# Optimization experiments

Measured on AMD Instinct MI355X. Metric: run time of the kernel, lower is better.

## Reference

```python
import jax, jax.numpy as jnp
import numpy as np

NUM_KNOTS = 10
DEGREE = 3
NUM_BASIS = NUM_KNOTS + DEGREE - 1  # 12
IN_FEATURES = 512
OUT_FEATURES = 512


def _interval_bounds():
    # t = linspace(0,1,num_knots); segment i covers [t[max(0,i-deg+1)], t[min(i+1,K-1)])
    t = np.linspace(0.0, 1.0, NUM_KNOTS, dtype=np.float32)
    idx = np.arange(NUM_BASIS)
    lower = t[np.maximum(0, idx - (DEGREE - 1))]
    upper = t[np.minimum(idx + 1, NUM_KNOTS - 1)]
    return jnp.asarray(lower), jnp.asarray(upper)


def setup_inputs() -> dict:
    key = jax.random.key(0)
    kx, kc = jax.random.split(key)
    x = jax.random.uniform(kx, (8, 2048, IN_FEATURES), dtype=jnp.float32)
    # coeffs for spline (i=out, j=in): torch indexes splines[i*in_features+j]
    coeffs = jax.random.normal(kc, (OUT_FEATURES, IN_FEATURES, NUM_BASIS), dtype=jnp.float32)
    return {"x": x, "coeffs": coeffs}


def reference(x, coeffs):
    lower, upper = _interval_bounds()  # [NUM_BASIS] each
    # piecewise-constant basis masks: [b, s, in, NUM_BASIS]
    xe = x[..., None]
    basis = ((xe >= lower) & (xe < upper)).astype(x.dtype)
    # out[b,s,i] = sum_j sum_k basis[b,s,j,k] * coeffs[i,j,k]
    return jnp.einsum("bsjk,ijk->bsi", basis, coeffs)
```

## Files before the change

kernel.cpp:

```cpp
#include <hip/hip_runtime.h>

#define MTOT 16384
#define NFEAT 512
#define KTOT 4608

typedef float f32x4 __attribute__((ext_vector_type(4)));
typedef short s16x8 __attribute__((ext_vector_type(8)));

__device__ __forceinline__ int div9(int c) { return (c * 7282) >> 16; }

#define GLDS(GP, LP) __builtin_amdgcn_global_load_lds( \
    (const __attribute__((address_space(1))) void*)(GP), \
    (__attribute__((address_space(3))) void*)(LP), 16, 0, 0)

__device__ __forceinline__ s16x8 decode_frag(unsigned code) {
  unsigned nb0 = code & 15u, nb1 = code >> 4;
  unsigned p0 = nb0 - 1u, p1 = nb1 - 1u;
  unsigned long long v0 = (nb0 ? 0x3F80ull : 0ull) << ((p0 & 3u) << 4);
  unsigned long long v1 = (nb1 ? 0x3F80ull : 0ull) << ((p1 & 3u) << 4);
  unsigned long long lo = (p0 < 4u ? v0 : 0ull) | (p1 < 4u ? v1 : 0ull);
  unsigned long long hi = (p0 < 4u ? 0ull : v0) | (p1 < 4u ? 0ull : v1);
  union { unsigned long long q[2]; s16x8 v; } u;
  u.q[0] = lo; u.q[1] = hi;
  return u.v;
}

__global__ __launch_bounds__(256) void prep(const float* __restrict__ x,
                                            const float* __restrict__ coeffs,
                                            unsigned char* __restrict__ codeT,
                                            unsigned short* __restrict__ Bmat) {
  __shared__ unsigned char segt[64][68];
  const int bx = blockIdx.x;
  const int tid = threadIdx.x;
  if (bx < 2048) {
    const int i = bx >> 2, q = bx & 3;
    const float* cb = coeffs + (size_t)i * 6144;
#pragma unroll
    for (int p = 0; p < 5; ++p) {
      int kl = p * 256 + tid;
      if (kl < 1152) {
        int k = q * 1152 + kl;
        int j = div9(k), s = k - j * 9;
        float v = cb[j * 12 + s] + cb[j * 12 + s + 1] + cb[j * 12 + s + 2];
        unsigned u = __float_as_uint(v);
        unsigned rn = (u + 0x7FFFu + ((u >> 16) & 1u)) >> 16;
        Bmat[(size_t)i * KTOT + k] = (unsigned short)rn;
      }
    }
  } else {
    const int bb = bx - 2048;
    const int mt = bb >> 3;
    const int jt = bb & 7;
    const int m0 = mt * 64;
    const float4* x4 = (const float4*)x;
    const float T1 = (float)(1.0/9.0), T2 = (float)(2.0/9.0), T3 = (float)(3.0/9.0),
                T4 = (float)(4.0/9.0), T5 = (float)(5.0/9.0), T6 = (float)(6.0/9.0),
                T7 = (float)(7.0/9.0), T8 = (float)(8.0/9.0);
#pragma unroll
    for (int it = 0; it < 4; ++it) {
      int f = it * 256 + tid;
      int m = f >> 4, jq = f & 15;
      float4 v = x4[(size_t)(m0 + m) * 128 + jt * 16 + jq];
      uchar4 sv;
      { float xv = v.x; sv.x = (unsigned char)((xv>=T1)+(xv>=T2)+(xv>=T3)+(xv>=T4)+(xv>=T5)+(xv>=T6)+(xv>=T7)+(xv>=T8)); }
      { float xv = v.y; sv.y = (unsigned char)((xv>=T1)+(xv>=T2)+(xv>=T3)+(xv>=T4)+(xv>=T5)+(xv>=T6)+(xv>=T7)+(xv>=T8)); }
      { float xv = v.z; sv.z = (unsigned char)((xv>=T1)+(xv>=T2)+(xv>=T3)+(xv>=T4)+(xv>=T5)+(xv>=T6)+(xv>=T7)+(xv>=T8)); }
      { float xv = v.w; sv.w = (unsigned char)((xv>=T1)+(xv>=T2)+(xv>=T3)+(xv>=T4)+(xv>=T5)+(xv>=T6)+(xv>=T7)+(xv>=T8)); }
      *(uchar4*)&segt[m][jq * 4] = sv;
    }
    __syncthreads();
#pragma unroll
    for (int p = 0; p < 5; ++p) {
      int u = p * 256 + tid;
      if (u < 1152) {
        int gl = u >> 4, mq = u & 15;
        int c0 = jt * 576 + gl * 8;
        int j0 = div9(c0), j1 = div9(c0 + 7);
        int j0l = j0 - jt * 64, j1l = j1 - jt * 64;
        uchar4 ob;
        unsigned char* pb = (unsigned char*)&ob;
#pragma unroll
        for (int c = 0; c < 4; ++c) {
          int m = mq + c * 16;
          int s0 = segt[m][j0l];
          int pos0 = j0 * 9 + s0 - c0;
          unsigned code = (pos0 >= 0 && pos0 < 8) ? (unsigned)(pos0 + 1) : 0u;
          if (j1 != j0) {
            int s1 = segt[m][j1l];
            int pos1 = j1 * 9 + s1 - c0;
            if (pos1 < 8) code |= (unsigned)(pos1 + 1) << 4;
          }
          pb[c] = (unsigned char)code;
        }
        *(uchar4*)(codeT + (size_t)(jt * 72 + gl) * MTOT + m0 + mq * 4) = ob;
      }
    }
  }
}

__global__ __launch_bounds__(256, 2) void kan_gemm(const unsigned char* __restrict__ codeT,
                                                   const unsigned short* __restrict__ Bmat,
                                                   float* __restrict__ out) {
  __shared__ __align__(16) short Blds[2][2][8192];
  const int tid = threadIdx.x;
  const int lane = tid & 63;
  const int wid = tid >> 6;
  const int mh = wid & 1;
  const int kh = wid >> 1;
  const int lm = lane & 15;
  const int lq = lane >> 4;
  const int bx = blockIdx.x;
  const int mt = bx >> 2;
  const int nt = bx & 3;
  const int m0 = mt * 128, n0 = nt * 128;
  const int mb64 = m0 + mh * 64;

  const unsigned short* gBp = Bmat + (size_t)(n0 + mh * 64 + lm) * KTOT + kh * 2304 + lq * 8;
  const unsigned* gC0 = (const unsigned*)(codeT + (size_t)(kh * 288 + lq) * MTOT + mb64) + lm;
  const unsigned* gC1 = (const unsigned*)(codeT + (size_t)(kh * 288 + 4 + lq) * MTOT + mb64) + lm;

  f32x4 acc[4][8] = {};
  s16x8 bfP[8], bfQ[8];
  unsigned crq[2][2];

#define CRLOAD(SET) do { \
    crq[SET][0] = gC0[0]; crq[SET][1] = gC1[0]; \
    gC0 += 2 * MTOT; gC1 += 2 * MTOT; } while (0)

#define ISSUE_B(SLOT) do { \
    short* dst = &Blds[kh][SLOT][mh * 4096]; \
    GLDS(gBp,                  dst);        \
    GLDS(gBp + 32,             dst + 512);  \
    GLDS(gBp + 16 * KTOT,      dst + 1024); \
    GLDS(gBp + 16 * KTOT + 32, dst + 1536); \
    GLDS(gBp + 32 * KTOT,      dst + 2048); \
    GLDS(gBp + 32 * KTOT + 32, dst + 2560); \
    GLDS(gBp + 48 * KTOT,      dst + 3072); \
    GLDS(gBp + 48 * KTOT + 32, dst + 3584); \
    gBp += 64; } while (0)

#define RD(BF, SLOT, KSD) do { \
    _Pragma("unroll") \
    for (int ns = 0; ns < 8; ++ns) \
      BF[ns] = *(const s16x8*)&Blds[kh][SLOT][(ns * 2 + (KSD)) * 512 + lane * 8]; \
    } while (0)

#define HALF(CRIDX, KSD, BF) do { \
    __builtin_amdgcn_s_setprio(1); \
    unsigned cw_ = crq[CRIDX][KSD]; \
    _Pragma("unroll") \
    for (int ms = 0; ms < 4; ++ms) { \
      s16x8 afv_ = decode_frag((cw_ >> (ms * 8)) & 255u); \
      _Pragma("unroll") \
      for (int ns = 0; ns < 8; ++ns) \
        acc[ms][ns] = __builtin_amdgcn_mfma_f32_16x16x32_bf16(afv_, BF[ns], acc[ms][ns], 0, 0, 0); \
    } \
    __builtin_amdgcn_s_setprio(0); } while (0)

#define VWAIT0() asm volatile("s_waitcnt vmcnt(0)" ::: "memory")
#define BAR()    __builtin_amdgcn_s_barrier()

  CRLOAD(0);
  ISSUE_B(0);
  VWAIT0();
  BAR();
  RD(bfP, 0, 0);

#pragma unroll 1
  for (int tt = 0; tt < 17; ++tt) {
    BAR();
    CRLOAD(1); ISSUE_B(1);
    RD(bfQ, 0, 1);
    HALF(0, 0, bfP);
    VWAIT0();
    BAR();
    RD(bfP, 1, 0);
    HALF(0, 1, bfQ);

    BAR();
    CRLOAD(0); ISSUE_B(0);
    RD(bfQ, 1, 1);
    HALF(1, 0, bfP);
    VWAIT0();
    BAR();
    RD(bfP, 0, 0);
    HALF(1, 1, bfQ);
  }

  BAR();
  CRLOAD(1); ISSUE_B(1);
  RD(bfQ, 0, 1);
  HALF(0, 0, bfP);
  VWAIT0();
  BAR();
  RD(bfP, 1, 0);
  HALF(0, 1, bfQ);

  BAR();
  RD(bfQ, 1, 1);
  HALF(1, 0, bfP);
  HALF(1, 1, bfQ);

  BAR();
  if (kh == 1) {
    float* p = (float*)(&Blds[0][0][0]) + mh * 8192;
#pragma unroll
    for (int ms = 0; ms < 4; ++ms)
#pragma unroll
      for (int ns = 0; ns < 8; ++ns)
#pragma unroll
        for (int rg = 0; rg < 4; ++rg)
          p[((ms * 8 + ns) * 4 + rg) * 64 + lane] = acc[ms][ns][rg];
  }
  __syncthreads();
  if (kh == 0) {
    const float* p = (const float*)(&Blds[0][0][0]) + mh * 8192;
#pragma unroll
    for (int ms = 0; ms < 4; ++ms)
#pragma unroll
      for (int ns = 0; ns < 8; ++ns) {
        int tok = mb64 + ms * 16 + lq * 4;
        int col = n0 + ns * 16 + lm;
        float* op = out + (size_t)tok * NFEAT + col;
#pragma unroll
        for (int rg = 0; rg < 4; ++rg)
          op[(size_t)rg * NFEAT] = acc[ms][ns][rg] + p[((ms * 8 + ns) * 4 + rg) * 64 + lane];
      }
  }
#undef CRLOAD
#undef ISSUE_B
#undef RD
#undef HALF
#undef VWAIT0
#undef BAR
}

extern "C" void kernel_launch(void* const* d_in, const int* in_sizes, int n_in,
                              void* d_out, int out_size, void* d_ws, size_t ws_size,
                              hipStream_t stream) {
  const float* x = (const float*)d_in[0];
  const float* coeffs = (const float*)d_in[1];
  float* out = (float*)d_out;
  unsigned char* codeT = (unsigned char*)d_ws;
  unsigned short* Bmat = (unsigned short*)((char*)d_ws + (size_t)576 * MTOT);

  prep<<<dim3(4096), dim3(256), 0, stream>>>(x, coeffs, codeT, Bmat);
  kan_gemm<<<dim3(512), dim3(256), 0, stream>>>(codeT, Bmat, out);
}
```

Baseline: 174.9 us.

## Split tile into barrier-fenced MFMA clusters interleaved with halved B loads

Each K-tile of the GEMM main loop is reorganized into four phases, each running 16 MFMAs. The global-to-LDS B load is split into two halves, and the next code-word load and LDS fragment reads are spread across those phases. Every phase is fenced by barriers and lgkmcnt waits. The aim is finer interleaving of memory traffic with matrix work across waves. The cost is many more barriers per tile and stricter wave synchronization, which could leave the MFMA pipe idle more often.

```diff
diff --git a/kernel.cpp b/kernel.cpp
--- a/kernel.cpp
+++ b/kernel.cpp
@@ -120,19 +120,22 @@
   const unsigned* gC1 = (const unsigned*)(codeT + (size_t)(kh * 288 + 4 + lq) * MTOT + mb64) + lm;
 
   f32x4 acc[4][8] = {};
-  s16x8 bfP[8], bfQ[8];
+  s16x8 bfA[8], bfB[8];
   unsigned crq[2][2];
 
 #define CRLOAD(SET) do { \
     crq[SET][0] = gC0[0]; crq[SET][1] = gC1[0]; \
     gC0 += 2 * MTOT; gC1 += 2 * MTOT; } while (0)
 
-#define ISSUE_B(SLOT) do { \
+#define ISSUE_B_A(SLOT) do { \
     short* dst = &Blds[kh][SLOT][mh * 4096]; \
     GLDS(gBp,                  dst);        \
     GLDS(gBp + 32,             dst + 512);  \
     GLDS(gBp + 16 * KTOT,      dst + 1024); \
-    GLDS(gBp + 16 * KTOT + 32, dst + 1536); \
+    GLDS(gBp + 16 * KTOT + 32, dst + 1536); } while (0)
+
+#define ISSUE_B_B(SLOT) do { \
+    short* dst = &Blds[kh][SLOT][mh * 4096]; \
     GLDS(gBp + 32 * KTOT,      dst + 2048); \
     GLDS(gBp + 32 * KTOT + 32, dst + 2560); \
     GLDS(gBp + 48 * KTOT,      dst + 3072); \
@@ -145,61 +148,72 @@
       BF[ns] = *(const s16x8*)&Blds[kh][SLOT][(ns * 2 + (KSD)) * 512 + lane * 8]; \
     } while (0)
 
-#define HALF(CRIDX, KSD, BF) do { \
+#define CLUSTER(CW, MSB, BF) do { \
     __builtin_amdgcn_s_setprio(1); \
-    unsigned cw_ = crq[CRIDX][KSD]; \
+    s16x8 a0_ = decode_frag(((CW) >> ((MSB) * 8)) & 255u); \
+    s16x8 a1_ = decode_frag(((CW) >> ((MSB) * 8 + 8)) & 255u); \
     _Pragma("unroll") \
-    for (int ms = 0; ms < 4; ++ms) { \
-      s16x8 afv_ = decode_frag((cw_ >> (ms * 8)) & 255u); \
-      _Pragma("unroll") \
-      for (int ns = 0; ns < 8; ++ns) \
-        acc[ms][ns] = __builtin_amdgcn_mfma_f32_16x16x32_bf16(afv_, BF[ns], acc[ms][ns], 0, 0, 0); \
-    } \
+    for (int ns = 0; ns < 8; ++ns) \
+      acc[(MSB)][ns] = __builtin_amdgcn_mfma_f32_16x16x32_bf16(a0_, BF[ns], acc[(MSB)][ns], 0, 0, 0); \
+    _Pragma("unroll") \
+    for (int ns = 0; ns < 8; ++ns) \
+      acc[(MSB) + 1][ns] = __builtin_amdgcn_mfma_f32_16x16x32_bf16(a1_, BF[ns], acc[(MSB) + 1][ns], 0, 0, 0); \
     __builtin_amdgcn_s_setprio(0); } while (0)
 
 #define VWAIT0() asm volatile("s_waitcnt vmcnt(0)" ::: "memory")
+#define LGKM0()  asm volatile("s_waitcnt lgkmcnt(0)" ::: "memory")
 #define BAR()    __builtin_amdgcn_s_barrier()
 
+#define TILE_FULL(S) do { \
+     \
+    ISSUE_B_A(S ^ 1); \
+    RD(bfB, S, 1); \
+    BAR(); LGKM0(); \
+    CLUSTER(crq[S][0], 0, bfA); \
+    BAR(); \
+     \
+    ISSUE_B_B(S ^ 1); \
+    BAR(); LGKM0(); \
+    CLUSTER(crq[S][0], 2, bfA); \
+    VWAIT0(); \
+    BAR(); \
+     \
+    RD(bfA, S ^ 1, 0); \
+    BAR(); LGKM0(); \
+    CLUSTER(crq[S][1], 0, bfB); \
+    BAR(); \
+     \
+    CRLOAD(S ^ 1); \
+    BAR(); LGKM0(); \
+    CLUSTER(crq[S][1], 2, bfB); \
+    BAR(); \
+  } while (0)
+
   CRLOAD(0);
-  ISSUE_B(0);
+  ISSUE_B_A(0);
+  ISSUE_B_B(0);
   VWAIT0();
   BAR();
-  RD(bfP, 0, 0);
+  RD(bfA, 0, 0);
 
 #pragma unroll 1
-  for (int tt = 0; tt < 17; ++tt) {
-    BAR();
-    CRLOAD(1); ISSUE_B(1);
-    RD(bfQ, 0, 1);
-    HALF(0, 0, bfP);
-    VWAIT0();
-    BAR();
-    RD(bfP, 1, 0);
-    HALF(0, 1, bfQ);
-
-    BAR();
-    CRLOAD(0); ISSUE_B(0);
-    RD(bfQ, 1, 1);
-    HALF(1, 0, bfP);
-    VWAIT0();
-    BAR();
-    RD(bfP, 0, 0);
-    HALF(1, 1, bfQ);
-  }
-
-  BAR();
-  CRLOAD(1); ISSUE_B(1);
-  RD(bfQ, 0, 1);
-  HALF(0, 0, bfP);
-  VWAIT0();
-  BAR();
-  RD(bfP, 1, 0);
-  HALF(0, 1, bfQ);
-
-  BAR();
-  RD(bfQ, 1, 1);
-  HALF(1, 0, bfP);
-  HALF(1, 1, bfQ);
+  for (int i = 0; i < 17; ++i) {
+    TILE_FULL(0);
+    TILE_FULL(1);
+  }
+  TILE_FULL(0);
+
+  RD(bfB, 1, 1);
+  BAR(); LGKM0();
+  CLUSTER(crq[1][0], 0, bfA);
+  BAR();
+  BAR(); LGKM0();
+  CLUSTER(crq[1][0], 2, bfA);
+  BAR();
+  BAR(); LGKM0();
+  CLUSTER(crq[1][1], 0, bfB);
+  BAR();
+  CLUSTER(crq[1][1], 2, bfB);
 
   BAR();
   if (kh == 1) {
@@ -228,11 +242,14 @@
       }
   }
 #undef CRLOAD
-#undef ISSUE_B
+#undef ISSUE_B_A
+#undef ISSUE_B_B
 #undef RD
-#undef HALF
+#undef CLUSTER
 #undef VWAIT0
+#undef LGKM0
 #undef BAR
+#undef TILE_FULL
 }
 
 extern "C" void kernel_launch(void* const* d_in, const int* in_sizes, int n_in,
```

New measurement: 182.2 us. 4.2% more time.
